# Performance work log

Hardware: AMD Instinct MI355X
Metric: run time of the kernel (lower is better)

## Reference

```python
import jax, jax.numpy as jnp
import numpy as np

N, D, B = 8192, 16, 4
F_EMB, F_FEAT, F_ENC, H, HID = 32, 4, 128, 4, 64
GRAPH_LAYERS, FLOW_ITERS, DUAL_ITERS = 2, 20, 20
DUAL_STEP, DUAL_MOM = 0.01, 0.9


def _graph():
    # symmetric circulant graph: offsets {1,N-1,2,N-2,...}; reverse of slot 2i is 2i+1
    offs = np.array([o for k in range(1, D // 2 + 1) for o in (k, N - k)], dtype=np.int32)
    rev = np.arange(D, dtype=np.int32).reshape(-1, 2)[:, ::-1].reshape(-1)
    v = np.arange(N, dtype=np.int32)[:, None]
    adj = (v + offs[None, :]) % N          # out-neighbor of node v at slot d
    in_nbr = (v - offs[None, :]) % N       # source node of in-edge to v stored at slot d
    out_flat = adj * D + rev[None, :]      # flat index of reverse edge in [N*D]
    bcast = lambda a: np.broadcast_to(a[None], (B, N, D)).copy()
    return bcast(adj), bcast(in_nbr), bcast(out_flat)


def setup_inputs() -> dict:
    key = jax.random.key(0)
    ks = iter(jax.random.split(key, 32))
    dense = lambda k, fi, fo: jax.random.normal(k, (fi, fo), jnp.float32) / np.sqrt(fi)
    adj, in_nbr, out_flat = _graph()
    demands = jax.random.normal(next(ks), (B, N, 1), jnp.float32)
    demands = demands - jnp.mean(demands, axis=1, keepdims=True)  # net-zero supply/demand
    return dict(
        node_embeddings=jax.random.normal(next(ks), (B, N, F_EMB), jnp.float32),
        node_features=jax.random.uniform(next(ks), (B, N, F_FEAT), jnp.float32),
        demands=demands,
        adj_lst=jnp.asarray(adj), flow_indices=jnp.asarray(in_nbr),
        out_indices=jnp.asarray(out_flat), num_nodes=N,
        enc_W1=dense(next(ks), F_EMB + F_FEAT, HID), enc_b1=jnp.zeros((HID,), jnp.float32),
        enc_W2=dense(next(ks), HID, F_ENC), enc_b2=jnp.zeros((F_ENC,), jnp.float32),
        attn_W=jax.random.normal(next(ks), (H, F_ENC, F_ENC), jnp.float32) / np.sqrt(F_ENC),
        attn_aq=jax.random.normal(next(ks), (H, F_ENC), jnp.float32) / np.sqrt(F_ENC),
        attn_ak=jax.random.normal(next(ks), (H, F_ENC), jnp.float32) / np.sqrt(F_ENC),
        gru_W=dense(next(ks), F_ENC, 3 * F_ENC), gru_U=dense(next(ks), F_ENC, 3 * F_ENC),
        gru_b=jnp.zeros((3 * F_ENC,), jnp.float32),
        dec_W1=dense(next(ks), F_ENC, HID), dec_b1=jnp.zeros((HID,), jnp.float32),
        dec_W2=dense(next(ks), HID, 1), dec_b2=jnp.zeros((1,), jnp.float32),
        dual_W1=dense(next(ks), F_ENC, HID), dual_b1=jnp.zeros((HID,), jnp.float32),
        dual_W2=dense(next(ks), HID, 1), dual_b2=jnp.zeros((1,), jnp.float32),
    )


def _mlp2(x, W1, b1, W2, b2, activate_final):
    h = jnp.tanh(x @ W1 + b1)
    o = h @ W2 + b2
    return jnp.tanh(o) if activate_final else o


def _attention_neighborhood(x, adj, W, aq, ak):
    # x:[B,N,F], adj:[B,N,D]; multi-head attention over adjacency-list neighbors
    cq = jnp.einsum('bnf,hf->bhn', x, jnp.einsum('hfg,hg->hf', W, aq))
    ck = jnp.einsum('bnf,hf->bhn', x, jnp.einsum('hfg,hg->hf', W, ak))
    ck_nb = jax.vmap(lambda c, a: c[:, a])(ck, adj)           # [B,H,N,D]
    attn = jax.nn.softmax(jnp.tanh(cq[..., None] + ck_nb), axis=-1)
    x_nb = jax.vmap(lambda xb, a: xb[a])(x, adj)              # [B,N,D,F]
    weighted = jnp.einsum('bhnd,bndf->bhnf', attn, x_nb)
    out = jnp.tanh(jnp.mean(jnp.einsum('bhnf,hfg->bhng', weighted, W), axis=1))
    return out, attn


def _gru(x, h, W, U, b):
    gz, gr, gc = jnp.split(x @ W + b, 3, axis=-1)
    Uz, Ur, Uc = jnp.split(U, 3, axis=1)
    z = jax.nn.sigmoid(gz + h @ Uz)
    r = jax.nn.sigmoid(gr + h @ Ur)
    c = jnp.tanh(gc + (r * h) @ Uc)
    return z * h + (1.0 - z) * c


def _cost(x):
    return x * x


def _cost_deriv(x):
    return 2.0 * x


def _mcf(w, demand, in_idx):
    # proportional min-cost-flow iteration; in_idx[b,v,d] = source of in-edge at slot d
    flow0 = w * jax.nn.relu(-demand)
    def step(carry, _):
        flow, _ = carry
        inflow = jnp.sum(jnp.take_along_axis(flow, in_idx, axis=1), axis=-1, keepdims=True)
        new = w * jax.nn.relu(inflow - demand)
        return (new, flow), None
    (flow, pflow), _ = jax.lax.scan(step, (flow0, flow0), None, length=FLOW_ITERS)
    return flow, pflow


def _dual_flow(dual_diff, mask):
    # projected momentum descent on cost(f) - dual_diff*f, f >= 0
    z = jnp.zeros_like(dual_diff)
    def step(carry, _):
        flow, acc = carry
        deriv = _cost_deriv(flow - DUAL_MOM * acc) - dual_diff
        acc2 = DUAL_MOM * acc + DUAL_STEP * deriv
        flow2 = jax.nn.relu(mask * (flow - acc2))
        return (flow2, acc2), None
    (flow, _), _ = jax.lax.scan(step, (z, z), None, length=DUAL_ITERS)
    return flow


def reference(node_embeddings, node_features, demands, adj_lst, flow_indices, out_indices,
              num_nodes, enc_W1, enc_b1, enc_W2, enc_b2, attn_W, attn_aq, attn_ak,
              gru_W, gru_U, gru_b, dec_W1, dec_b1, dec_W2, dec_b2,
              dual_W1, dual_b1, dual_W2, dual_b2):
    h = _mlp2(jnp.concatenate([node_embeddings, node_features], axis=-1),
              enc_W1, enc_b1, enc_W2, enc_b2, True)
    for _ in range(GRAPH_LAYERS):  # layers share weights (tf AUTO_REUSE)
        nxt, _ = _attention_neighborhood(h, adj_lst, attn_W, attn_aq, attn_ak)
        h = _gru(nxt, h, gru_W, gru_U, gru_b)
    node_w = _mlp2(h, dec_W1, dec_b1, dec_W2, dec_b2, False)       # [B,N,1]
    pred = jax.vmap(lambda w, a: w[a, 0])(node_w, adj_lst)         # [B,N,D]
    mask = (adj_lst != num_nodes).astype(pred.dtype)
    norm_w = jax.nn.softmax(pred, axis=-1)
    flow, _ = _mcf(norm_w, demands, flow_indices)
    # flow correction: cancel opposing flow on reverse edges
    bf = flow.reshape(B, N * D)
    rev = jnp.take_along_axis(bf, out_indices.reshape(B, N * D), axis=1).reshape(flow.shape)
    flow = jax.nn.relu(flow - jnp.minimum(flow, rev))
    flow_cost = jnp.sum(_cost(flow), axis=(1, 2))
    dual_vars = _mlp2(h, dual_W1, dual_b1, dual_W2, dual_b2, False)  # [B,N,1]
    dual = mask * dual_vars
    dual_tr = mask * jax.vmap(lambda w, a: w[a, 0])(dual_vars, adj_lst)
    dual_diff = dual - dual_tr
    dual_flows = _dual_flow(dual_diff, mask)
    dual_demand = jnp.sum(dual_vars * demands, axis=(1, 2))
    dual_cost = jnp.sum(_cost(dual_flows) - dual_diff * dual_flows, axis=(1, 2)) - dual_demand
    return flow_cost - dual_cost  # loss, [B]
```

## Files before the change

### kernel.cpp

```cpp
#include <hip/hip_runtime.h>

#define NN 8192
#define BB 4
#define DD 16

typedef unsigned short ushort_t;
typedef short bf16x8 __attribute__((ext_vector_type(8)));
typedef float f32x4 __attribute__((ext_vector_type(4)));
typedef unsigned short u16x4 __attribute__((ext_vector_type(4)));

__host__ __device__ constexpr int soff(int d) { return (d & 1) ? -((d >> 1) + 1) : ((d >> 1) + 1); }

__device__ __forceinline__ float sigmoidf(float x) { return 1.f / (1.f + expf(-x)); }

__device__ __forceinline__ unsigned short f2b(float f) {
  union { float f; unsigned int u; } x;
  x.f = f;
  unsigned int r = (x.u + 0x7FFFu + ((x.u >> 16) & 1u)) >> 16;
  return (unsigned short)r;
}
__device__ __forceinline__ float b2f(ushort_t v) {
  union { unsigned int u; float f; } x;
  x.u = ((unsigned int)v) << 16;
  return x.f;
}

__device__ __forceinline__ float wave_sum(float v) {
#pragma unroll
  for (int o = 32; o; o >>= 1) v += __shfl_down(v, o, 64);
  return v;
}

__global__ __launch_bounds__(256) void prep_kernel(
    const float* __restrict__ gW, const float* __restrict__ gU, const float* __restrict__ aW,
    const float* __restrict__ eW1, const float* __restrict__ eW2,
    const float* __restrict__ dW1, const float* __restrict__ uW1,
    ushort_t* __restrict__ Wt, ushort_t* __restrict__ Wt3, ushort_t* __restrict__ Wt2,
    ushort_t* __restrict__ W1f, ushort_t* __restrict__ W2f,
    ushort_t* __restrict__ dW1f, ushort_t* __restrict__ uW1f) {
  int i = blockIdx.x * 256 + threadIdx.x;
  if (i < 98304) {
    int e = i & 7, lane = (i >> 3) & 63, ks = (i >> 9) & 7, nt = i >> 12;
    int m = lane & 15, g = lane >> 4;
    int n = nt * 16 + m, k = ks * 32 + g * 8 + e;
    float v;
    if (k < 128) v = gW[k * 384 + n];
    else v = (n < 256) ? gU[(k - 128) * 384 + n] : 0.f;
    Wt[i] = f2b(v);
  } else if (i < 114688) {
    int j = i - 98304;
    int e = j & 7, lane = (j >> 3) & 63, ks = (j >> 9) & 3, nt = j >> 11;
    int m = lane & 15, g = lane >> 4;
    int n = nt * 16 + m, k = ks * 32 + g * 8 + e;
    Wt3[j] = f2b(gU[k * 384 + 256 + n]);
  } else if (i < 180224) {
    int j = i - 114688;
    int e = j & 7, lane = (j >> 3) & 63, ks = (j >> 9) & 15, nt = j >> 13;
    int m = lane & 15, g = lane >> 4;
    int gc = nt * 16 + m, k = ks * 32 + g * 8 + e;
    int hh = k >> 7, f = k & 127;
    Wt2[j] = f2b(aW[hh * 16384 + f * 128 + gc]);
  } else if (i < 184320) {
    int j = i - 180224;
    int e = j & 7, lane = (j >> 3) & 63, ks = (j >> 9) & 1, nt = j >> 10;
    int m = lane & 15, g = lane >> 4;
    int n = nt * 16 + m, k = ks * 32 + g * 8 + e;
    W1f[j] = f2b(k < 36 ? eW1[k * 64 + n] : 0.f);
  } else if (i < 192512) {
    int j = i - 184320;
    int e = j & 7, lane = (j >> 3) & 63, ks = (j >> 9) & 1, nt = j >> 10;
    int m = lane & 15, g = lane >> 4;
    int n = nt * 16 + m, k = ks * 32 + g * 8 + e;
    W2f[j] = f2b(eW2[k * 128 + n]);
  } else if (i < 200704) {
    int j = i - 192512;
    int e = j & 7, lane = (j >> 3) & 63, ks = (j >> 9) & 3, nt = j >> 11;
    int m = lane & 15, g = lane >> 4;
    int n = nt * 16 + m, k = ks * 32 + g * 8 + e;
    dW1f[j] = f2b(dW1[k * 64 + n]);
  } else if (i < 208896) {
    int j = i - 200704;
    int e = j & 7, lane = (j >> 3) & 63, ks = (j >> 9) & 3, nt = j >> 11;
    int m = lane & 15, g = lane >> 4;
    int n = nt * 16 + m, k = ks * 32 + g * 8 + e;
    uW1f[j] = f2b(uW1[k * 64 + n]);
  }
}

#define EBS 72
__global__ __launch_bounds__(256) void enc_kernel(
    const float* __restrict__ emb, const float* __restrict__ feat,
    const ushort_t* __restrict__ W1f, const float* __restrict__ b1,
    const ushort_t* __restrict__ W2f, const float* __restrict__ b2,
    float* __restrict__ hout) {
  __shared__ alignas(16) ushort_t embB[64 * EBS];
  __shared__ alignas(16) ushort_t hidB[64 * EBS];
  int tid = threadIdx.x;
  int w = tid >> 6, lane = tid & 63, m = lane & 15, g = lane >> 4;
  size_t n0 = (size_t)blockIdx.x * 64;
  f32x4 z4 = {0.f, 0.f, 0.f, 0.f};
#pragma unroll
  for (int i = 0; i < 9; i++) ((unsigned int*)embB)[tid + i * 256] = 0u;
  __syncthreads();
#pragma unroll
  for (int i = 0; i < 2; i++) {
    int idx = tid + i * 256;
    int r = idx >> 3, c4 = (idx & 7) * 4;
    float4 v = *(const float4*)&emb[(n0 + r) * 32 + c4];
    u16x4 q = {f2b(v.x), f2b(v.y), f2b(v.z), f2b(v.w)};
    *(u16x4*)&embB[r * EBS + c4] = q;
  }
  if (tid < 64) {
    float4 v = *(const float4*)&feat[(n0 + tid) * 4];
    u16x4 q = {f2b(v.x), f2b(v.y), f2b(v.z), f2b(v.w)};
    *(u16x4*)&embB[tid * EBS + 32] = q;
  }
  __syncthreads();
  {
    f32x4 acc[4];
#pragma unroll
    for (int nt = 0; nt < 4; nt++) acc[nt] = z4;
#pragma unroll
    for (int ks = 0; ks < 2; ks++) {
      bf16x8 a = *(const bf16x8*)&embB[(w * 16 + m) * EBS + ks * 32 + g * 8];
#pragma unroll
      for (int nt = 0; nt < 4; nt++) {
        bf16x8 bb = *(const bf16x8*)&W1f[((nt * 2 + ks) * 64 + lane) * 8];
        acc[nt] = __builtin_amdgcn_mfma_f32_16x16x32_bf16(a, bb, acc[nt], 0, 0, 0);
      }
    }
#pragma unroll
    for (int nt = 0; nt < 4; nt++) {
      int col = nt * 16 + m;
      float bv = b1[col];
#pragma unroll
      for (int r = 0; r < 4; r++)
        hidB[(w * 16 + g * 4 + r) * EBS + col] = f2b(tanhf(acc[nt][r] + bv));
    }
  }
  __syncthreads();
  {
    f32x4 acc[8];
#pragma unroll
    for (int nt = 0; nt < 8; nt++) acc[nt] = z4;
#pragma unroll
    for (int ks = 0; ks < 2; ks++) {
      bf16x8 a = *(const bf16x8*)&hidB[(w * 16 + m) * EBS + ks * 32 + g * 8];
#pragma unroll
      for (int nt = 0; nt < 8; nt++) {
        bf16x8 bb = *(const bf16x8*)&W2f[((nt * 2 + ks) * 64 + lane) * 8];
        acc[nt] = __builtin_amdgcn_mfma_f32_16x16x32_bf16(a, bb, acc[nt], 0, 0, 0);
      }
    }
#pragma unroll
    for (int nt = 0; nt < 8; nt++) {
      int col = nt * 16 + m;
      float bv = b2[col];
#pragma unroll
      for (int r = 0; r < 4; r++)
        hout[(n0 + w * 16 + g * 4 + r) * 128 + col] = tanhf(acc[nt][r] + bv);
    }
  }
}

__global__ __launch_bounds__(256) void aqw_kernel(
    const float* __restrict__ W, const float* __restrict__ aq, const float* __restrict__ ak,
    ushort_t* __restrict__ aqkB) {
  int i = blockIdx.x * 256 + threadIdx.x;
  if (i < 512) {
    int hh = i >> 7, f = i & 127;
    const float* w = W + ((size_t)hh * 128 + f) * 128;
    float s = 0.f, s2 = 0.f;
    for (int g = 0; g < 128; g++) {
      s += w[g] * aq[hh * 128 + g];
      s2 += w[g] * ak[hh * 128 + g];
    }
    int ks = f >> 5, g = (f >> 3) & 3, e = f & 7;
    aqkB[(ks * 64 + g * 16 + hh) * 8 + e] = f2b(s2);
    aqkB[(ks * 64 + g * 16 + 4 + hh) * 8 + e] = f2b(s);
  } else if (i < 2560) {
    int j = i - 512;
    int lane = (j >> 3) & 63;
    if ((lane & 15) >= 8) aqkB[j] = 0;
  }
}

#define HBS 136
#define HTS 40
#define WGS 520
#define HSS 136
__global__ __launch_bounds__(256, 4) void layer_kernel(
    const float* __restrict__ hin, const ushort_t* __restrict__ Wt2,
    const ushort_t* __restrict__ Wt, const ushort_t* __restrict__ Wt3,
    const ushort_t* __restrict__ aqkB,
    const float* __restrict__ bg, float* __restrict__ hout) {
  __shared__ alignas(16) ushort_t hl_bf[32 * HBS];
  __shared__ alignas(16) ushort_t hlT_u[128 * HTS];
  __shared__ float ckl[32 * 5];
  __shared__ float cql[16 * 5];
  __shared__ alignas(16) ushort_t aexp[4 * 16 * 32];
  __shared__ alignas(16) ushort_t wgB[16 * WGS];
  ushort_t* hlT = hlT_u;
  ushort_t* xB = hlT_u;
  ushort_t* rhB = hlT_u + 16 * HBS;
  int b = blockIdx.y, v0 = blockIdx.x * 16, tid = threadIdx.x;
  int w = tid >> 6, lane = tid & 63, m = lane & 15, g = lane >> 4;
  const float* hb = hin + (size_t)b * NN * 128;
  size_t base = ((size_t)b * NN + v0) * 128;
  f32x4 z4 = {0.f, 0.f, 0.f, 0.f};
#pragma unroll
  for (int i = 0; i < 4; i++) {
    int idx = tid + i * 256;
    int r = idx >> 5, c4 = (idx & 31) * 4;
    int row = (v0 - 8 + r) & (NN - 1);
    float4 v = *(const float4*)&hb[(size_t)row * 128 + c4];
    u16x4 q = {f2b(v.x), f2b(v.y), f2b(v.z), f2b(v.w)};
    *(u16x4*)&hl_bf[r * HBS + c4] = q;
  }
#pragma unroll
  for (int i = 0; i < 4; i++) ((unsigned int*)aexp)[tid + i * 256] = 0u;
  __syncthreads();
#pragma unroll
  for (int i = 0; i < 4; i++) {
    int idx = tid + i * 256;
    int c = idx & 127, r4 = (idx >> 7) * 4;
    u16x4 q = {hl_bf[r4 * HBS + c], hl_bf[(r4 + 1) * HBS + c],
               hl_bf[(r4 + 2) * HBS + c], hl_bf[(r4 + 3) * HBS + c]};
    *(u16x4*)&hlT[c * HTS + r4] = q;
  }
  if (w < 2) {
    f32x4 accB = z4;
    for (int ks = 0; ks < 4; ks++) {
      bf16x8 a = *(const bf16x8*)&hl_bf[(w * 16 + m) * HBS + ks * 32 + g * 8];
      bf16x8 bb = *(const bf16x8*)&aqkB[(ks * 64 + lane) * 8];
      accB = __builtin_amdgcn_mfma_f32_16x16x32_bf16(a, bb, accB, 0, 0, 0);
    }
    int arow = w * 16 + g * 4;
    if (m < 4) {
#pragma unroll
      for (int r = 0; r < 4; r++) ckl[(arow + r) * 5 + m] = accB[r];
    } else if (m < 8) {
#pragma unroll
      for (int r = 0; r < 4; r++) {
        int row = arow + r;
        if (row >= 8 && row < 24) cql[(row - 8) * 5 + (m - 4)] = accB[r];
      }
    }
  }
  __syncthreads();
  if (tid < 64) {
    int t = tid >> 2, hh = tid & 3;
    float ex[16];
    float mx = -3.0e38f;
    float cq = cql[t * 5 + hh];
#pragma unroll
    for (int d = 0; d < 16; d++) {
      float s = tanhf(cq + ckl[(t + 8 + soff(d)) * 5 + hh]);
      ex[d] = s;
      mx = fmaxf(mx, s);
    }
    float sum = 0.f;
#pragma unroll
    for (int d = 0; d < 16; d++) {
      ex[d] = expf(ex[d] - mx);
      sum += ex[d];
    }
    float inv = 1.f / sum;
#pragma unroll
    for (int d = 0; d < 16; d++)
      aexp[(hh * 16 + t) * 32 + (t + 8 + soff(d))] = f2b(ex[d] * inv);
  }
  __syncthreads();
#pragma unroll
  for (int hh = 0; hh < 4; hh++) {
    bf16x8 a = *(const bf16x8*)&aexp[(hh * 16 + m) * 32 + g * 8];
#pragma unroll
    for (int t2 = 0; t2 < 2; t2++) {
      int nt = w * 2 + t2;
      bf16x8 bb = *(const bf16x8*)&hlT[(nt * 16 + m) * HTS + g * 8];
      f32x4 c = __builtin_amdgcn_mfma_f32_16x16x32_bf16(a, bb, z4, 0, 0, 0);
#pragma unroll
      for (int r = 0; r < 4; r++)
        wgB[(g * 4 + r) * WGS + hh * 128 + nt * 16 + m] = f2b(c[r]);
    }
  }
  __syncthreads();
  {
    f32x4 acc[2];
    acc[0] = z4; acc[1] = z4;
    for (int ks = 0; ks < 16; ks++) {
      bf16x8 a = *(const bf16x8*)&wgB[m * WGS + ks * 32 + g * 8];
#pragma unroll
      for (int t2 = 0; t2 < 2; t2++) {
        int nt = w * 2 + t2;
        bf16x8 bb = *(const bf16x8*)&Wt2[((nt * 16 + ks) * 64 + lane) * 8];
        acc[t2] = __builtin_amdgcn_mfma_f32_16x16x32_bf16(a, bb, acc[t2], 0, 0, 0);
      }
    }
    __syncthreads();
#pragma unroll
    for (int t2 = 0; t2 < 2; t2++) {
      int gc = (w * 2 + t2) * 16 + m;
#pragma unroll
      for (int r = 0; r < 4; r++)
        xB[(g * 4 + r) * HBS + gc] = f2b(tanhf(0.25f * acc[t2][r]));
    }
  }
  __syncthreads();
  f32x4 accZ[2], accR[2], accG[2];
#pragma unroll
  for (int t2 = 0; t2 < 2; t2++) { accZ[t2] = z4; accR[t2] = z4; accG[t2] = z4; }
  for (int ks = 0; ks < 8; ks++) {
    bf16x8 a = (ks < 4) ? *(const bf16x8*)&xB[m * HBS + ks * 32 + g * 8]
                        : *(const bf16x8*)&hl_bf[(m + 8) * HBS + (ks - 4) * 32 + g * 8];
#pragma unroll
    for (int t2 = 0; t2 < 2; t2++) {
      int ntz = w * 2 + t2;
      bf16x8 bz = *(const bf16x8*)&Wt[((ntz * 8 + ks) * 64 + lane) * 8];
      accZ[t2] = __builtin_amdgcn_mfma_f32_16x16x32_bf16(a, bz, accZ[t2], 0, 0, 0);
      bf16x8 br = *(const bf16x8*)&Wt[(((8 + ntz) * 8 + ks) * 64 + lane) * 8];
      accR[t2] = __builtin_amdgcn_mfma_f32_16x16x32_bf16(a, br, accR[t2], 0, 0, 0);
      if (ks < 4) {
        bf16x8 bc = *(const bf16x8*)&Wt[(((16 + ntz) * 8 + ks) * 64 + lane) * 8];
        accG[t2] = __builtin_amdgcn_mfma_f32_16x16x32_bf16(a, bc, accG[t2], 0, 0, 0);
      }
    }
  }
  float zf[2][4], gcf[2][4];
#pragma unroll
  for (int t2 = 0; t2 < 2; t2++) {
    int j = (w * 2 + t2) * 16 + m;
    float bz = bg[j], br = bg[128 + j], bc = bg[256 + j];
#pragma unroll
    for (int r = 0; r < 4; r++) {
      int row = g * 4 + r;
      float hv = b2f(hl_bf[(row + 8) * HBS + j]);
      zf[t2][r] = sigmoidf(accZ[t2][r] + bz);
      float rr = sigmoidf(accR[t2][r] + br);
      rhB[row * HBS + j] = f2b(rr * hv);
      gcf[t2][r] = accG[t2][r] + bc;
    }
  }
  __syncthreads();
  float* hstage = (float*)wgB;
  {
    f32x4 acc2[2];
    acc2[0] = z4; acc2[1] = z4;
    for (int ks = 0; ks < 4; ks++) {
      bf16x8 a = *(const bf16x8*)&rhB[m * HBS + ks * 32 + g * 8];
#pragma unroll
      for (int t2 = 0; t2 < 2; t2++) {
        int nt = w * 2 + t2;
        bf16x8 bb = *(const bf16x8*)&Wt3[((nt * 4 + ks) * 64 + lane) * 8];
        acc2[t2] = __builtin_amdgcn_mfma_f32_16x16x32_bf16(a, bb, acc2[t2], 0, 0, 0);
      }
    }
#pragma unroll
    for (int t2 = 0; t2 < 2; t2++) {
      int j = (w * 2 + t2) * 16 + m;
#pragma unroll
      for (int r = 0; r < 4; r++) {
        int row = g * 4 + r;
        float hv = b2f(hl_bf[(row + 8) * HBS + j]);
        float c = tanhf(gcf[t2][r] + acc2[t2][r]);
        hstage[row * HSS + j] = zf[t2][r] * hv + (1.f - zf[t2][r]) * c;
      }
    }
  }
  __syncthreads();
#pragma unroll
  for (int i = 0; i < 2; i++) {
    int idx = tid + i * 256;
    int row = idx >> 5, c4 = (idx & 31) * 4;
    *(float4*)&hout[base + (size_t)row * 128 + c4] = *(const float4*)&hstage[row * HSS + c4];
  }
}

__global__ __launch_bounds__(256) void dec_kernel(
    const float* __restrict__ h, const float* __restrict__ dem,
    const ushort_t* __restrict__ dW1f, const float* __restrict__ db1,
    const float* __restrict__ dW2, const float* __restrict__ db2,
    const ushort_t* __restrict__ uW1f, const float* __restrict__ ub1,
    const float* __restrict__ uW2, const float* __restrict__ ub2,
    float* __restrict__ node_w, float* __restrict__ dual_v, float* __restrict__ acc) {
  __shared__ alignas(16) ushort_t hB[64 * HBS];
  __shared__ float red[4];
  int b = blockIdx.y, n0 = blockIdx.x * 64, tid = threadIdx.x;
  int w = tid >> 6, lane = tid & 63, m = lane & 15, g = lane >> 4;
  f32x4 z4 = {0.f, 0.f, 0.f, 0.f};
  size_t base = ((size_t)b * NN + n0) * 128;
#pragma unroll
  for (int i = 0; i < 8; i++) {
    int idx = tid + i * 256;
    int r = idx >> 5, c4 = (idx & 31) * 4;
    float4 v = *(const float4*)&h[base + (size_t)r * 128 + c4];
    u16x4 q = {f2b(v.x), f2b(v.y), f2b(v.z), f2b(v.w)};
    *(u16x4*)&hB[r * HBS + c4] = q;
  }
  __syncthreads();
  f32x4 accD[4], accU[4];
#pragma unroll
  for (int nt = 0; nt < 4; nt++) { accD[nt] = z4; accU[nt] = z4; }
  for (int ks = 0; ks < 4; ks++) {
    bf16x8 a = *(const bf16x8*)&hB[(w * 16 + m) * HBS + ks * 32 + g * 8];
#pragma unroll
    for (int nt = 0; nt < 4; nt++) {
      bf16x8 bd = *(const bf16x8*)&dW1f[((nt * 4 + ks) * 64 + lane) * 8];
      accD[nt] = __builtin_amdgcn_mfma_f32_16x16x32_bf16(a, bd, accD[nt], 0, 0, 0);
      bf16x8 bu = *(const bf16x8*)&uW1f[((nt * 4 + ks) * 64 + lane) * 8];
      accU[nt] = __builtin_amdgcn_mfma_f32_16x16x32_bf16(a, bu, accU[nt], 0, 0, 0);
    }
  }
  float accd = 0.f;
#pragma unroll
  for (int r = 0; r < 4; r++) {
    float sD = 0.f, sU = 0.f;
#pragma unroll
    for (int nt = 0; nt < 4; nt++) {
      int col = nt * 16 + m;
      sD += tanhf(accD[nt][r] + db1[col]) * dW2[col];
      sU += tanhf(accU[nt][r] + ub1[col]) * uW2[col];
    }
#pragma unroll
    for (int o = 1; o < 16; o <<= 1) {
      sD += __shfl_xor(sD, o, 64);
      sU += __shfl_xor(sU, o, 64);
    }
    if (m == 0) {
      int n = n0 + w * 16 + g * 4 + r;
      node_w[(size_t)b * NN + n] = sD + db2[0];
      float dv = sU + ub2[0];
      dual_v[(size_t)b * NN + n] = dv;
      accd += dv * dem[(size_t)b * NN + n];
    }
  }
  float s = wave_sum(accd);
  if (lane == 0) red[w] = s;
  __syncthreads();
  if (tid == 0) atomicAdd(&acc[b], red[0] + red[1] + red[2] + red[3]);
}

__global__ __launch_bounds__(256) void sm_kernel(
    const float* __restrict__ node_w, const float* __restrict__ dem,
    float* __restrict__ nwT, float* __restrict__ fl0) {
  int b = blockIdx.y;
  int v = blockIdx.x * 256 + threadIdx.x;
  const float* nw = node_w + (size_t)b * NN;
  float p[16];
  float mx = -3.0e38f;
#pragma unroll
  for (int d = 0; d < 16; d++) {
    p[d] = nw[(v + soff(d)) & (NN - 1)];
    mx = fmaxf(mx, p[d]);
  }
  float s = 0.f;
#pragma unroll
  for (int d = 0; d < 16; d++) {
    p[d] = expf(p[d] - mx);
    s += p[d];
  }
  float inv = 1.f / s;
  float fd = fmaxf(-dem[(size_t)b * NN + v], 0.f);
#pragma unroll
  for (int d = 0; d < 16; d++) {
    size_t idx = ((size_t)b * 16 + d) * NN + v;
    float w = p[d] * inv;
    nwT[idx] = w;
    fl0[idx] = w * fd;
  }
}

#define MCI 10
#define MHALO 80
#define MCOLS (256 + 2 * MHALO)
__global__ __launch_bounds__(256) void mcf_fused_kernel(
    const float* __restrict__ src, float* __restrict__ dstg,
    const float* __restrict__ nwT, const float* __restrict__ dem) {
  __shared__ float fl[2][16][MCOLS];
  __shared__ float dm[MCOLS];
  int b = blockIdx.y, v0 = blockIdx.x * 256, tid = threadIdx.x;
  for (int e = tid; e < 16 * MCOLS; e += 256) {
    int d = e / MCOLS, c = e - d * MCOLS;
    int g = (v0 - MHALO + c) & (NN - 1);
    fl[0][d][c] = src[((size_t)b * 16 + d) * NN + g];
  }
  for (int c = tid; c < MCOLS; c += 256)
    dm[c] = dem[(size_t)b * NN + ((v0 - MHALO + c) & (NN - 1))];
  __syncthreads();
  int cur = 0;
  for (int it = 0; it < MCI; it++) {
    int lo = 8 * (it + 1), hi = MCOLS - 8 * (it + 1);
    for (int c = lo + tid; c < hi; c += 256) {
      float s = 0.f;
#pragma unroll
      for (int d = 0; d < 16; d++) s += fl[cur][d][c - soff(d)];
      float val = fmaxf(s - dm[c], 0.f);
      int g = (v0 - MHALO + c) & (NN - 1);
#pragma unroll
      for (int d = 0; d < 16; d++)
        fl[1 - cur][d][c] = nwT[((size_t)b * 16 + d) * NN + g] * val;
    }
    cur ^= 1;
    __syncthreads();
  }
  {
    int c = MHALO + tid;
    int g = v0 + tid;
#pragma unroll
    for (int d = 0; d < 16; d++)
      dstg[((size_t)b * 16 + d) * NN + g] = fl[cur][d][c];
  }
}

__global__ __launch_bounds__(256) void cost_kernel(const float* __restrict__ fl, float* __restrict__ acc) {
  __shared__ float red[4];
  int b = blockIdx.y;
  int v = blockIdx.x * 256 + threadIdx.x;
  float s = 0.f;
#pragma unroll
  for (int d = 0; d < 16; d++) {
    float f = fl[((size_t)b * 16 + d) * NN + v];
    int a = (v + soff(d)) & (NN - 1);
    float r = fl[((size_t)b * 16 + (d ^ 1)) * NN + a];
    float c = f - fminf(f, r);
    c = fmaxf(c, 0.f);
    s += c * c;
  }
  s = wave_sum(s);
  int lane = threadIdx.x & 63, wid = threadIdx.x >> 6;
  if (lane == 0) red[wid] = s;
  __syncthreads();
  if (threadIdx.x == 0) atomicAdd(&acc[b], red[0] + red[1] + red[2] + red[3]);
}

__global__ __launch_bounds__(256) void dual_kernel(const float* __restrict__ dv, float* __restrict__ acc) {
  __shared__ float red[4];
  int b = blockIdx.y;
  int v = blockIdx.x * 256 + threadIdx.x;
  float me = dv[(size_t)b * NN + v];
  float s = 0.f;
#pragma unroll
  for (int d = 0; d < 16; d++) {
    float dd = me - dv[(size_t)b * NN + ((v + soff(d)) & (NN - 1))];
    float f = 0.f, ac = 0.f;
#pragma unroll
    for (int it = 0; it < 20; it++) {
      float deriv = 2.f * (f - 0.9f * ac) - dd;
      ac = 0.9f * ac + 0.01f * deriv;
      f = fmaxf(f - ac, 0.f);
    }
    s += f * f - dd * f;
  }
  s = wave_sum(s);
  int lane = threadIdx.x & 63, wid = threadIdx.x >> 6;
  if (lane == 0) red[wid] = s;
  __syncthreads();
  if (threadIdx.x == 0) atomicAdd(&acc[b], -(red[0] + red[1] + red[2] + red[3]));
}

__global__ __launch_bounds__(64) void fin_kernel(const float* __restrict__ acc, float* __restrict__ out) {
  int i = threadIdx.x;
  if (i < BB) out[i] = acc[i];
}
__global__ __launch_bounds__(64) void sentinel_kernel(float* __restrict__ out) {
  int i = threadIdx.x;
  if (i < BB) out[i] = 99999.0f;
}

extern "C" void kernel_launch(void* const* d_in, const int* in_sizes, int n_in,
                              void* d_out, int out_size, void* d_ws, size_t ws_size,
                              hipStream_t stream) {
  (void)out_size; (void)ws_size;
  float* out = (float*)d_out;
  if (n_in < 25 || in_sizes[0] != 1048576 || in_sizes[3] != 524288 ||
      in_sizes[11] != 65536 || in_sizes[14] != 49152 || in_sizes[24] != 1) {
    sentinel_kernel<<<dim3(1), 64, 0, stream>>>(out);
    return;
  }
  const float* emb = (const float*)d_in[0];
  const float* feat = (const float*)d_in[1];
  const float* dem = (const float*)d_in[2];
  const float* eW1 = (const float*)d_in[7];
  const float* eb1 = (const float*)d_in[8];
  const float* eW2 = (const float*)d_in[9];
  const float* eb2 = (const float*)d_in[10];
  const float* aW = (const float*)d_in[11];
  const float* aq = (const float*)d_in[12];
  const float* ak = (const float*)d_in[13];
  const float* gW = (const float*)d_in[14];
  const float* gU = (const float*)d_in[15];
  const float* gb = (const float*)d_in[16];
  const float* dW1 = (const float*)d_in[17];
  const float* db1 = (const float*)d_in[18];
  const float* dW2 = (const float*)d_in[19];
  const float* db2 = (const float*)d_in[20];
  const float* uW1 = (const float*)d_in[21];
  const float* ub1 = (const float*)d_in[22];
  const float* uW2 = (const float*)d_in[23];
  const float* ub2 = (const float*)d_in[24];

  float* ws = (float*)d_ws;
  float* h = ws;
  float* h2 = h + 4194304;
  float* aqkBf = h2 + 4194304;
  float* node_w = aqkBf + 1024;
  float* dualv = node_w + 32768;
  float* nwT = dualv + 32768;
  float* flA = nwT + 524288;
  float* flB = flA + 524288;
  ushort_t* aqkB = (ushort_t*)aqkBf;
  float* acc = aqkBf;
  ushort_t* Wt = (ushort_t*)nwT;
  ushort_t* Wt3 = Wt + 98304;
  ushort_t* Wt2 = Wt3 + 16384;
  ushort_t* W1f = Wt2 + 65536;
  ushort_t* W2f = W1f + 4096;
  ushort_t* dW1f = W2f + 8192;
  ushort_t* uW1f = dW1f + 8192;

  aqw_kernel<<<dim3(10), 256, 0, stream>>>(aW, aq, ak, aqkB);
  prep_kernel<<<dim3(816), 256, 0, stream>>>(gW, gU, aW, eW1, eW2, dW1, uW1,
                                             Wt, Wt3, Wt2, W1f, W2f, dW1f, uW1f);
  enc_kernel<<<dim3(512), 256, 0, stream>>>(emb, feat, W1f, eb1, W2f, eb2, h);
  layer_kernel<<<dim3(512, 4), 256, 0, stream>>>(h, Wt2, Wt, Wt3, aqkB, gb, h2);
  layer_kernel<<<dim3(512, 4), 256, 0, stream>>>(h2, Wt2, Wt, Wt3, aqkB, gb, h);
  hipMemsetAsync(acc, 0, BB * sizeof(float), stream);
  dec_kernel<<<dim3(128, 4), 256, 0, stream>>>(h, dem, dW1f, db1, dW2, db2,
                                               uW1f, ub1, uW2, ub2, node_w, dualv, acc);
  sm_kernel<<<dim3(32, 4), 256, 0, stream>>>(node_w, dem, nwT, flA);
  mcf_fused_kernel<<<dim3(32, 4), 256, 0, stream>>>(flA, flB, nwT, dem);
  mcf_fused_kernel<<<dim3(32, 4), 256, 0, stream>>>(flB, flA, nwT, dem);
  cost_kernel<<<dim3(32, 4), 256, 0, stream>>>(flA, acc);
  dual_kernel<<<dim3(32, 4), 256, 0, stream>>>(dualv, acc);
  fin_kernel<<<dim3(1), 64, 0, stream>>>(acc, out);
}
```

Before: 167.2 us.

## Store hidden states as bf16, spread softmax across threads, shrink small-kernel blocks

Hidden-state buffers between encoder, graph layers and decoder are now stored as bf16 instead of fp32. This halves global traffic for the large [B,N,128] tensors and removes per-load conversions. The attention softmax now uses all 256 threads, four per (node, head), with shuffle reductions instead of 64 threads each looping over 16. The small tail kernels (sm, mcf, cost, dual) use smaller blocks and more of them to fill more CUs, at the cost of more redundant halo loads in mcf and more atomics. Rounding the stored h to bf16 adds some precision loss, though the layers already converted it to bf16 before use.

Result: faster. 158.7 us (-5.1%).

```diff
diff --git a/kernel.cpp b/kernel.cpp
--- a/kernel.cpp
+++ b/kernel.cpp
@@ -8,6 +8,7 @@
 typedef short bf16x8 __attribute__((ext_vector_type(8)));
 typedef float f32x4 __attribute__((ext_vector_type(4)));
 typedef unsigned short u16x4 __attribute__((ext_vector_type(4)));
+typedef unsigned short u16x8 __attribute__((ext_vector_type(8)));
 
 __host__ __device__ constexpr int soff(int d) { return (d & 1) ? -((d >> 1) + 1) : ((d >> 1) + 1); }
 
@@ -92,7 +93,7 @@
     const float* __restrict__ emb, const float* __restrict__ feat,
     const ushort_t* __restrict__ W1f, const float* __restrict__ b1,
     const ushort_t* __restrict__ W2f, const float* __restrict__ b2,
-    float* __restrict__ hout) {
+    ushort_t* __restrict__ hout) {
   __shared__ alignas(16) ushort_t embB[64 * EBS];
   __shared__ alignas(16) ushort_t hidB[64 * EBS];
   int tid = threadIdx.x;
@@ -158,7 +159,7 @@
       float bv = b2[col];
 #pragma unroll
       for (int r = 0; r < 4; r++)
-        hout[(n0 + w * 16 + g * 4 + r) * 128 + col] = tanhf(acc[nt][r] + bv);
+        hout[(n0 + w * 16 + g * 4 + r) * 128 + col] = f2b(tanhf(acc[nt][r] + bv));
     }
   }
 }
@@ -188,12 +189,11 @@
 #define HBS 136
 #define HTS 40
 #define WGS 520
-#define HSS 136
 __global__ __launch_bounds__(256, 4) void layer_kernel(
-    const float* __restrict__ hin, const ushort_t* __restrict__ Wt2,
+    const ushort_t* __restrict__ hin, const ushort_t* __restrict__ Wt2,
     const ushort_t* __restrict__ Wt, const ushort_t* __restrict__ Wt3,
     const ushort_t* __restrict__ aqkB,
-    const float* __restrict__ bg, float* __restrict__ hout) {
+    const float* __restrict__ bg, ushort_t* __restrict__ hout) {
   __shared__ alignas(16) ushort_t hl_bf[32 * HBS];
   __shared__ alignas(16) ushort_t hlT_u[128 * HTS];
   __shared__ float ckl[32 * 5];
@@ -205,17 +205,15 @@
   ushort_t* rhB = hlT_u + 16 * HBS;
   int b = blockIdx.y, v0 = blockIdx.x * 16, tid = threadIdx.x;
   int w = tid >> 6, lane = tid & 63, m = lane & 15, g = lane >> 4;
-  const float* hb = hin + (size_t)b * NN * 128;
+  const ushort_t* hb = hin + (size_t)b * NN * 128;
   size_t base = ((size_t)b * NN + v0) * 128;
   f32x4 z4 = {0.f, 0.f, 0.f, 0.f};
 #pragma unroll
-  for (int i = 0; i < 4; i++) {
+  for (int i = 0; i < 2; i++) {
     int idx = tid + i * 256;
-    int r = idx >> 5, c4 = (idx & 31) * 4;
+    int r = idx >> 4, c8 = (idx & 15) * 8;
     int row = (v0 - 8 + r) & (NN - 1);
-    float4 v = *(const float4*)&hb[(size_t)row * 128 + c4];
-    u16x4 q = {f2b(v.x), f2b(v.y), f2b(v.z), f2b(v.w)};
-    *(u16x4*)&hl_bf[r * HBS + c4] = q;
+    *(u16x8*)&hl_bf[r * HBS + c8] = *(const u16x8*)&hb[(size_t)row * 128 + c8];
   }
 #pragma unroll
   for (int i = 0; i < 4; i++) ((unsigned int*)aexp)[tid + i * 256] = 0u;
@@ -248,27 +246,35 @@
     }
   }
   __syncthreads();
-  if (tid < 64) {
-    int t = tid >> 2, hh = tid & 3;
-    float ex[16];
+  {
+    int grp = tid >> 2, q = tid & 3;
+    int t = grp >> 2, hh = grp & 3;
+    float cq = cql[t * 5 + hh];
+    float ex[4];
     float mx = -3.0e38f;
-    float cq = cql[t * 5 + hh];
-#pragma unroll
-    for (int d = 0; d < 16; d++) {
+#pragma unroll
+    for (int dq = 0; dq < 4; dq++) {
+      int d = q * 4 + dq;
       float s = tanhf(cq + ckl[(t + 8 + soff(d)) * 5 + hh]);
-      ex[d] = s;
+      ex[dq] = s;
       mx = fmaxf(mx, s);
     }
+    mx = fmaxf(mx, __shfl_xor(mx, 1, 64));
+    mx = fmaxf(mx, __shfl_xor(mx, 2, 64));
     float sum = 0.f;
 #pragma unroll
-    for (int d = 0; d < 16; d++) {
-      ex[d] = expf(ex[d] - mx);
-      sum += ex[d];
-    }
+    for (int dq = 0; dq < 4; dq++) {
+      ex[dq] = expf(ex[dq] - mx);
+      sum += ex[dq];
+    }
+    sum += __shfl_xor(sum, 1, 64);
+    sum += __shfl_xor(sum, 2, 64);
     float inv = 1.f / sum;
 #pragma unroll
-    for (int d = 0; d < 16; d++)
-      aexp[(hh * 16 + t) * 32 + (t + 8 + soff(d))] = f2b(ex[d] * inv);
+    for (int dq = 0; dq < 4; dq++) {
+      int d = q * 4 + dq;
+      aexp[(hh * 16 + t) * 32 + (t + 8 + soff(d))] = f2b(ex[dq] * inv);
+    }
   }
   __syncthreads();
 #pragma unroll
@@ -342,7 +348,7 @@
     }
   }
   __syncthreads();
-  float* hstage = (float*)wgB;
+  ushort_t* hstage = wgB;
   {
     f32x4 acc2[2];
     acc2[0] = z4; acc2[1] = z4;
@@ -363,21 +369,19 @@
         int row = g * 4 + r;
         float hv = b2f(hl_bf[(row + 8) * HBS + j]);
         float c = tanhf(gcf[t2][r] + acc2[t2][r]);
-        hstage[row * HSS + j] = zf[t2][r] * hv + (1.f - zf[t2][r]) * c;
+        hstage[row * HBS + j] = f2b(zf[t2][r] * hv + (1.f - zf[t2][r]) * c);
       }
     }
   }
   __syncthreads();
-#pragma unroll
-  for (int i = 0; i < 2; i++) {
-    int idx = tid + i * 256;
-    int row = idx >> 5, c4 = (idx & 31) * 4;
-    *(float4*)&hout[base + (size_t)row * 128 + c4] = *(const float4*)&hstage[row * HSS + c4];
+  {
+    int row = tid >> 4, c8 = (tid & 15) * 8;
+    *(u16x8*)&hout[base + (size_t)row * 128 + c8] = *(const u16x8*)&hstage[row * HBS + c8];
   }
 }
 
 __global__ __launch_bounds__(256) void dec_kernel(
-    const float* __restrict__ h, const float* __restrict__ dem,
+    const ushort_t* __restrict__ h, const float* __restrict__ dem,
     const ushort_t* __restrict__ dW1f, const float* __restrict__ db1,
     const float* __restrict__ dW2, const float* __restrict__ db2,
     const ushort_t* __restrict__ uW1f, const float* __restrict__ ub1,
@@ -390,12 +394,10 @@
   f32x4 z4 = {0.f, 0.f, 0.f, 0.f};
   size_t base = ((size_t)b * NN + n0) * 128;
 #pragma unroll
-  for (int i = 0; i < 8; i++) {
+  for (int i = 0; i < 4; i++) {
     int idx = tid + i * 256;
-    int r = idx >> 5, c4 = (idx & 31) * 4;
-    float4 v = *(const float4*)&h[base + (size_t)r * 128 + c4];
-    u16x4 q = {f2b(v.x), f2b(v.y), f2b(v.z), f2b(v.w)};
-    *(u16x4*)&hB[r * HBS + c4] = q;
+    int r = idx >> 4, c8 = (idx & 15) * 8;
+    *(u16x8*)&hB[r * HBS + c8] = *(const u16x8*)&h[base + (size_t)r * 128 + c8];
   }
   __syncthreads();
   f32x4 accD[4], accU[4];
@@ -440,11 +442,11 @@
   if (tid == 0) atomicAdd(&acc[b], red[0] + red[1] + red[2] + red[3]);
 }
 
-__global__ __launch_bounds__(256) void sm_kernel(
+__global__ __launch_bounds__(64) void sm_kernel(
     const float* __restrict__ node_w, const float* __restrict__ dem,
     float* __restrict__ nwT, float* __restrict__ fl0) {
   int b = blockIdx.y;
-  int v = blockIdx.x * 256 + threadIdx.x;
+  int v = blockIdx.x * 64 + threadIdx.x;
   const float* nw = node_w + (size_t)b * NN;
   float p[16];
   float mx = -3.0e38f;
@@ -472,13 +474,14 @@
 
 #define MCI 10
 #define MHALO 80
-#define MCOLS (256 + 2 * MHALO)
+#define MCW 128
+#define MCOLS (MCW + 2 * MHALO)
 __global__ __launch_bounds__(256) void mcf_fused_kernel(
     const float* __restrict__ src, float* __restrict__ dstg,
     const float* __restrict__ nwT, const float* __restrict__ dem) {
   __shared__ float fl[2][16][MCOLS];
   __shared__ float dm[MCOLS];
-  int b = blockIdx.y, v0 = blockIdx.x * 256, tid = threadIdx.x;
+  int b = blockIdx.y, v0 = blockIdx.x * MCW, tid = threadIdx.x;
   for (int e = tid; e < 16 * MCOLS; e += 256) {
     int d = e / MCOLS, c = e - d * MCOLS;
     int g = (v0 - MHALO + c) & (NN - 1);
@@ -503,7 +506,7 @@
     cur ^= 1;
     __syncthreads();
   }
-  {
+  if (tid < MCW) {
     int c = MHALO + tid;
     int g = v0 + tid;
 #pragma unroll
@@ -512,10 +515,9 @@
   }
 }
 
-__global__ __launch_bounds__(256) void cost_kernel(const float* __restrict__ fl, float* __restrict__ acc) {
-  __shared__ float red[4];
+__global__ __launch_bounds__(64) void cost_kernel(const float* __restrict__ fl, float* __restrict__ acc) {
   int b = blockIdx.y;
-  int v = blockIdx.x * 256 + threadIdx.x;
+  int v = blockIdx.x * 64 + threadIdx.x;
   float s = 0.f;
 #pragma unroll
   for (int d = 0; d < 16; d++) {
@@ -527,16 +529,12 @@
     s += c * c;
   }
   s = wave_sum(s);
-  int lane = threadIdx.x & 63, wid = threadIdx.x >> 6;
-  if (lane == 0) red[wid] = s;
-  __syncthreads();
-  if (threadIdx.x == 0) atomicAdd(&acc[b], red[0] + red[1] + red[2] + red[3]);
-}
-
-__global__ __launch_bounds__(256) void dual_kernel(const float* __restrict__ dv, float* __restrict__ acc) {
-  __shared__ float red[4];
+  if (threadIdx.x == 0) atomicAdd(&acc[b], s);
+}
+
+__global__ __launch_bounds__(64) void dual_kernel(const float* __restrict__ dv, float* __restrict__ acc) {
   int b = blockIdx.y;
-  int v = blockIdx.x * 256 + threadIdx.x;
+  int v = blockIdx.x * 64 + threadIdx.x;
   float me = dv[(size_t)b * NN + v];
   float s = 0.f;
 #pragma unroll
@@ -552,10 +550,7 @@
     s += f * f - dd * f;
   }
   s = wave_sum(s);
-  int lane = threadIdx.x & 63, wid = threadIdx.x >> 6;
-  if (lane == 0) red[wid] = s;
-  __syncthreads();
-  if (threadIdx.x == 0) atomicAdd(&acc[b], -(red[0] + red[1] + red[2] + red[3]));
+  if (threadIdx.x == 0) atomicAdd(&acc[b], -s);
 }
 
 __global__ __launch_bounds__(64) void fin_kernel(const float* __restrict__ acc, float* __restrict__ out) {
@@ -600,9 +595,9 @@
   const float* ub2 = (const float*)d_in[24];
 
   float* ws = (float*)d_ws;
-  float* h = ws;
-  float* h2 = h + 4194304;
-  float* aqkBf = h2 + 4194304;
+  ushort_t* h = (ushort_t*)ws;
+  ushort_t* h2 = h + 4194304;
+  float* aqkBf = ws + 4194304;
   float* node_w = aqkBf + 1024;
   float* dualv = node_w + 32768;
   float* nwT = dualv + 32768;
@@ -627,10 +622,10 @@
   hipMemsetAsync(acc, 0, BB * sizeof(float), stream);
   dec_kernel<<<dim3(128, 4), 256, 0, stream>>>(h, dem, dW1f, db1, dW2, db2,
                                                uW1f, ub1, uW2, ub2, node_w, dualv, acc);
-  sm_kernel<<<dim3(32, 4), 256, 0, stream>>>(node_w, dem, nwT, flA);
-  mcf_fused_kernel<<<dim3(32, 4), 256, 0, stream>>>(flA, flB, nwT, dem);
-  mcf_fused_kernel<<<dim3(32, 4), 256, 0, stream>>>(flB, flA, nwT, dem);
-  cost_kernel<<<dim3(32, 4), 256, 0, stream>>>(flA, acc);
-  dual_kernel<<<dim3(32, 4), 256, 0, stream>>>(dualv, acc);
+  sm_kernel<<<dim3(128, 4), 64, 0, stream>>>(node_w, dem, nwT, flA);
+  mcf_fused_kernel<<<dim3(64, 4), 256, 0, stream>>>(flA, flB, nwT, dem);
+  mcf_fused_kernel<<<dim3(64, 4), 256, 0, stream>>>(flB, flA, nwT, dem);
+  cost_kernel<<<dim3(128, 4), 64, 0, stream>>>(flA, acc);
+  dual_kernel<<<dim3(128, 4), 64, 0, stream>>>(dualv, acc);
   fin_kernel<<<dim3(1), 64, 0, stream>>>(acc, out);
 }
```
